# Kernel optimization log

Hardware: AMD Instinct MI355X
Metric: run time of the kernel (lower is better)

## Reference

```python
import jax, jax.numpy as jnp
import numpy as np

D_MODEL = 1024
N_HEADS = 16
HEAD_DIM = D_MODEL // N_HEADS
N_SCALES = 11
_D4 = jnp.array([0.4829629131445341, 0.8365163037378079, 0.2241438680420134, -0.1294095225512604], dtype=jnp.float32)


def setup_inputs() -> dict:
    key = jax.random.key(0)
    ks = jax.random.split(key, 8)
    B, N, D = 8, 2048, D_MODEL
    s = 1.0 / np.sqrt(D)
    x = jax.random.normal(ks[0], (B, N, D), dtype=jnp.float32)
    qkv_w = jax.random.normal(ks[1], (3 * D, D), dtype=jnp.float32) * s
    qkv_b = jnp.zeros((3 * D,), dtype=jnp.float32)
    out_w = jax.random.normal(ks[2], (D, D), dtype=jnp.float32) * s
    out_b = jnp.zeros((D,), dtype=jnp.float32)
    gate_w = jax.random.normal(ks[3], (D, D), dtype=jnp.float32) * s
    gate_b = jnp.full((D,), 2.0, dtype=jnp.float32)  # nn.init.constant_(gate_proj.bias, 2.0)
    scale_gain = jax.random.normal(ks[4], (N_SCALES, N_HEADS), dtype=jnp.float32) * 0.1
    field_coupling = jnp.eye(N_HEADS, dtype=jnp.float32) + 0.01 * jax.random.normal(ks[5], (N_HEADS, N_HEADS), dtype=jnp.float32)
    return {"x": x, "qkv_w": qkv_w, "qkv_b": qkv_b, "out_w": out_w, "out_b": out_b,
            "gate_w": gate_w, "gate_b": gate_b, "scale_gain": scale_gain,
            "field_coupling": field_coupling}


def _causal_multiscale(x_c, scale_gain):
    # x_c: [B, C, N] with channel order (head-major, then head_dim)
    B, C, N = x_c.shape
    gains = jax.nn.softmax(scale_gain, axis=0)              # [S, H]
    gains_exp = jnp.repeat(gains, HEAD_DIM, axis=1)         # [S, C]
    out = jnp.zeros_like(x_c)
    for j in range(N_SCALES):
        d = 1 << j
        xp = jnp.pad(x_c, ((0, 0), (0, 0), (3 * d, 0)))     # causal left pad
        # depthwise dilated conv (cross-correlation, same D4 taps per channel)
        y = (_D4[0] * xp[:, :, 0 * d:0 * d + N]
             + _D4[1] * xp[:, :, 1 * d:1 * d + N]
             + _D4[2] * xp[:, :, 2 * d:2 * d + N]
             + _D4[3] * xp[:, :, 3 * d:3 * d + N])
        out = out + gains_exp[j][None, :, None] * y
    return out


def reference(x, qkv_w, qkv_b, out_w, out_b, gate_w, gate_b, scale_gain, field_coupling):
    B, N, D = x.shape
    H, HD = N_HEADS, HEAD_DIM
    qkv = x @ qkv_w.T + qkv_b                               # [B, N, 3D]
    q, k, v = jnp.split(qkv, 3, axis=-1)                    # q is unused (as in source)
    k = k.reshape(B, N, H, HD)
    v = v.reshape(B, N, H, HD)
    k_mag = jnp.linalg.norm(k, axis=-1, keepdims=True)      # [B, N, H, 1]
    field = v * k_mag                                       # [B, N, H, HD]
    # -> [B, C, N], C = H*HD, head-major channel layout
    x_c = jnp.transpose(field, (0, 2, 3, 1)).reshape(B, H * HD, N)
    out_c = _causal_multiscale(x_c, scale_gain)             # [B, C, N]
    field = out_c.reshape(B, H, HD, N)                      # [B, H, HD, N]
    coupling = jax.nn.softmax(field_coupling, axis=-1)      # [H, H]
    field = jnp.einsum('ij,bjdn->bidn', coupling, field)    # head coupling
    gathered = jnp.transpose(field, (0, 3, 1, 2)).reshape(B, N, D)
    gate = jax.nn.sigmoid(x @ gate_w.T + gate_b)
    return (gathered * gate) @ out_w.T + out_b
```

## Files before the change

kernel.cpp:

```cpp
#include <hip/hip_runtime.h>
#include <hip/hip_bf16.h>
#include <math.h>

#define BD 8
#define SN 2048
#define DM 1024
#define NH 16
#define HD 64
#define NS 11
#define NTAP 24
#define PAD 3072

typedef __attribute__((ext_vector_type(8))) short short8;
typedef __attribute__((ext_vector_type(4))) float floatx4;

__constant__ int OFFS[NTAP] = {0, 1, 2, 3, 4, 6, 8, 12, 16, 24, 32, 48, 64, 96,
                               128, 192, 256, 384, 512, 768, 1024, 1536, 2048, 3072};

__device__ __forceinline__ void async_load16(const void* g, void* lds) {
    __builtin_amdgcn_global_load_lds(
        (const __attribute__((address_space(1))) void*)g,
        (__attribute__((address_space(3))) void*)lds,
        16, 0, 0);
}

__global__ __launch_bounds__(256) void f2bf_kernel(const float* __restrict__ src,
                                                   __hip_bfloat16* __restrict__ dst,
                                                   int n4) {
    int i = blockIdx.x * 256 + threadIdx.x;
    if (i < n4) {
        const float4 v = reinterpret_cast<const float4*>(src)[i];
        union { __hip_bfloat16 h[4]; uint2 u; } cv;
        cv.h[0] = __float2bfloat16(v.x);
        cv.h[1] = __float2bfloat16(v.y);
        cv.h[2] = __float2bfloat16(v.z);
        cv.h[3] = __float2bfloat16(v.w);
        reinterpret_cast<uint2*>(dst)[i] = cv.u;
    }
}

__global__ void prep_kernel(const float* __restrict__ scale_gain,
                            const float* __restrict__ field_coupling,
                            float* __restrict__ wtab,
                            float* __restrict__ cw) {
    const float D4[4] = {0.4829629131445341f, 0.8365163037378079f,
                         0.2241438680420134f, -0.1294095225512604f};
    int t = threadIdx.x;
    if (t < NH) {
        float g[NS];
        float m = -1e30f;
        for (int j = 0; j < NS; ++j) m = fmaxf(m, scale_gain[j * NH + t]);
        float s = 0.f;
        for (int j = 0; j < NS; ++j) { g[j] = expf(scale_gain[j * NH + t] - m); s += g[j]; }
        float inv = 1.f / s;
        for (int j = 0; j < NS; ++j) g[j] *= inv;
        for (int i = 0; i < NTAP; ++i) {
            float w = 0.f;
            for (int j = 0; j < NS; ++j)
                for (int tt = 0; tt < 4; ++tt)
                    if (((3 - tt) << j) == OFFS[i]) w += g[j] * D4[tt];
            wtab[i * NH + t] = w;
        }
    } else if (t < 2 * NH) {
        int r = t - NH;
        float m = -1e30f;
        for (int j = 0; j < NH; ++j) m = fmaxf(m, field_coupling[r * NH + j]);
        float e[NH]; float s = 0.f;
        for (int j = 0; j < NH; ++j) { e[j] = expf(field_coupling[r * NH + j] - m); s += e[j]; }
        float inv = 1.f / s;
        for (int j = 0; j < NH; ++j) cw[r * NH + j] = e[j] * inv;
    }
}

__global__ __launch_bounds__(256, 3) void gemm128_kernel(
    const __hip_bfloat16* __restrict__ A,
    const __hip_bfloat16* __restrict__ Bw,
    void* __restrict__ Cout,
    const float* __restrict__ bias,
    int M, int Nn, int K, int act, int bf16out) {
    __shared__ short As[128 * 64];
    __shared__ short Bs[128 * 64];

    const int tid = threadIdx.x;
    const int m0 = blockIdx.y * 128;
    const int n0 = blockIdx.x * 128;
    const int wv = tid >> 6;
    const int ln = tid & 63;

    const int srow = ln >> 3;
    const int scc  = (ln & 7) ^ srow;
    size_t goffA[4], goffB[4];
    #pragma unroll
    for (int i = 0; i < 4; ++i) {
        const int row = wv * 32 + i * 8 + srow;
        goffA[i] = (size_t)(m0 + row) * K + scc * 8;
        goffB[i] = (size_t)(n0 + row) * K + scc * 8;
    }

    const int lrow = ln & 15, quad = ln >> 4;
    const int wm = (wv >> 1) * 64;
    const int wn = (wv & 1) * 64;
    int aaddr[4], baddr[4];
    #pragma unroll
    for (int t = 0; t < 4; ++t) {
        const int sw = (quad ^ (lrow & 7)) * 16;
        aaddr[t] = (wm + t * 16 + lrow) * 128 + sw;
        baddr[t] = (wn + t * 16 + lrow) * 128 + sw;
    }

    floatx4 acc[4][4];
    #pragma unroll
    for (int a = 0; a < 4; ++a)
        #pragma unroll
        for (int b = 0; b < 4; ++b) acc[a][b] = (floatx4){0.f, 0.f, 0.f, 0.f};

    for (int kt = 0; kt < K; kt += 64) {
        #pragma unroll
        for (int i = 0; i < 4; ++i) {
            async_load16(A + goffA[i] + kt, &As[(wv * 32 + i * 8) * 64]);
            async_load16(Bw + goffB[i] + kt, &Bs[(wv * 32 + i * 8) * 64]);
        }
        __syncthreads();
        #pragma unroll
        for (int h = 0; h < 2; ++h) {
            short8 a[4], b[4];
            #pragma unroll
            for (int t = 0; t < 4; ++t) {
                a[t] = *reinterpret_cast<const short8*>(
                           reinterpret_cast<const char*>(As) + (aaddr[t] ^ (h * 64)));
                b[t] = *reinterpret_cast<const short8*>(
                           reinterpret_cast<const char*>(Bs) + (baddr[t] ^ (h * 64)));
            }
            #pragma unroll
            for (int mt = 0; mt < 4; ++mt)
                #pragma unroll
                for (int nt = 0; nt < 4; ++nt)
                    acc[mt][nt] = __builtin_amdgcn_mfma_f32_16x16x32_bf16(
                        a[mt], b[nt], acc[mt][nt], 0, 0, 0);
        }
        __syncthreads();
    }

    #pragma unroll
    for (int mt = 0; mt < 4; ++mt) {
        #pragma unroll
        for (int nt = 0; nt < 4; ++nt) {
            const int col = n0 + wn + nt * 16 + lrow;
            const float bv = bias ? bias[col] : 0.f;
            #pragma unroll
            for (int i = 0; i < 4; ++i) {
                const int row = m0 + wm + mt * 16 + quad * 4 + i;
                float val = acc[mt][nt][i] + bv;
                if (act == 1) val = 1.f / (1.f + expf(-val));
                if (bf16out)
                    ((__hip_bfloat16*)Cout)[(size_t)row * Nn + col] = __float2bfloat16(val);
                else
                    ((float*)Cout)[(size_t)row * Nn + col] = val;
            }
        }
    }
}

__global__ __launch_bounds__(256) void fieldize_kernel(const __hip_bfloat16* __restrict__ kv,
                                                       __hip_bfloat16* __restrict__ field) {
    const int b = blockIdx.z, h = blockIdx.y, n0 = blockIdx.x * 64;
    __shared__ float kt[64][65];
    __shared__ float vt[64][65];
    __shared__ float mag[64];
    const int t = threadIdx.x;
    #pragma unroll
    for (int i = 0; i < 16; ++i) {
        int idx = t + i * 256;
        int nl = idx >> 6, d = idx & 63;
        size_t rbase = (size_t)(b * SN + n0 + nl) * 2048;
        kt[nl][d] = __bfloat162float(kv[rbase + h * 64 + d]);
        vt[nl][d] = __bfloat162float(kv[rbase + 1024 + h * 64 + d]);
    }
    __syncthreads();
    if (t < 64) {
        float s = 0.f;
        #pragma unroll
        for (int d = 0; d < 64; ++d) { float x = kt[t][d]; s += x * x; }
        mag[t] = sqrtf(s);
    }
    __syncthreads();
    #pragma unroll
    for (int i = 0; i < 16; ++i) {
        int idx = t + i * 256;
        int d = idx >> 6, nl = idx & 63;
        field[((size_t)b * DM + h * 64 + d) * SN + n0 + nl] =
            __float2bfloat16(vt[nl][d] * mag[nl]);
    }
}

__global__ __launch_bounds__(256) void wavelet_kernel(const __hip_bfloat16* __restrict__ field,
                                                      const float* __restrict__ wtab,
                                                      __hip_bfloat16* __restrict__ wave) {
    const int bc = blockIdx.x;
    const int c = bc & (DM - 1);
    const int h = c >> 6;
    __shared__ float row[PAD + SN];
    __shared__ float wt[NTAP];
    const __hip_bfloat16* src = field + (size_t)bc * SN;
    const int t = threadIdx.x;
    for (int i = t; i < PAD; i += 256) row[i] = 0.f;
    for (int i = t; i < SN; i += 256) row[PAD + i] = __bfloat162float(src[i]);
    if (t < NTAP) wt[t] = wtab[t * NH + h];
    __syncthreads();
    __hip_bfloat16* dst = wave + (size_t)bc * SN;
    for (int n = t; n < SN; n += 256) {
        const float* base = &row[PAD + n];
        float acc = 0.f;
        #pragma unroll
        for (int i = 0; i < NTAP; ++i) acc += wt[i] * base[-OFFS[i]];
        dst[n] = __float2bfloat16(acc);
    }
}

__global__ __launch_bounds__(256) void couple_kernel(const __hip_bfloat16* __restrict__ wave,
                                                     const float* __restrict__ cw,
                                                     __hip_bfloat16* __restrict__ cpl) {
    const int b = blockIdx.z, d = blockIdx.y;
    const int n = blockIdx.x * 256 + threadIdx.x;
    __shared__ float w[256];
    w[threadIdx.x] = cw[threadIdx.x];
    __syncthreads();
    size_t base = (size_t)b * DM * SN + (size_t)d * SN + n;
    float r[NH];
    #pragma unroll
    for (int hi = 0; hi < NH; ++hi) r[hi] = __bfloat162float(wave[base + (size_t)hi * 64 * SN]);
    #pragma unroll
    for (int ho = 0; ho < NH; ++ho) {
        float acc = 0.f;
        #pragma unroll
        for (int hi = 0; hi < NH; ++hi) acc += w[ho * 16 + hi] * r[hi];
        cpl[base + (size_t)ho * 64 * SN] = __float2bfloat16(acc);
    }
}

__global__ __launch_bounds__(256) void transgate_kernel(const __hip_bfloat16* __restrict__ cpl,
                                                        const __hip_bfloat16* __restrict__ gate,
                                                        __hip_bfloat16* __restrict__ Ag) {
    const int b = blockIdx.z;
    const int c0 = blockIdx.y * 64, n0 = blockIdx.x * 64;
    __shared__ float tile[64][65];
    const int t = threadIdx.x;
    #pragma unroll
    for (int i = 0; i < 16; ++i) {
        int idx = t + i * 256;
        int ci = idx >> 6, nj = idx & 63;
        tile[ci][nj] = __bfloat162float(cpl[((size_t)b * DM + c0 + ci) * SN + n0 + nj]);
    }
    __syncthreads();
    #pragma unroll
    for (int i = 0; i < 16; ++i) {
        int idx = t + i * 256;
        int nj = idx >> 6, ci = idx & 63;
        size_t off = ((size_t)(b * SN + n0 + nj)) * DM + c0 + ci;
        Ag[off] = __float2bfloat16(tile[ci][nj] * __bfloat162float(gate[off]));
    }
}

extern "C" void kernel_launch(void* const* d_in, const int* in_sizes, int n_in,
                              void* d_out, int out_size, void* d_ws, size_t ws_size,
                              hipStream_t stream) {
    const float* x     = (const float*)d_in[0];
    const float* qkv_w = (const float*)d_in[1];
    const float* qkv_b = (const float*)d_in[2];
    const float* out_w = (const float*)d_in[3];
    const float* out_b = (const float*)d_in[4];
    const float* gate_w = (const float*)d_in[5];
    const float* gate_b = (const float*)d_in[6];
    const float* scale_gain = (const float*)d_in[7];
    const float* field_coupling = (const float*)d_in[8];

    char* ws = (char*)d_ws;
    const int M = BD * SN;

    __hip_bfloat16* x_bf   = (__hip_bfloat16*)(ws);
    __hip_bfloat16* wkv_bf = (__hip_bfloat16*)(ws + 33554432);
    __hip_bfloat16* wg_bf  = (__hip_bfloat16*)(ws + 37748736);
    __hip_bfloat16* wo_bf  = (__hip_bfloat16*)(ws + 39845888);
    float* wtab            = (float*)(ws + 41943040);
    float* cwbuf           = (float*)(ws + 41944576);
    __hip_bfloat16* gate_bf  = (__hip_bfloat16*)(ws + 41945600);
    __hip_bfloat16* field_bf = (__hip_bfloat16*)(ws + 75500032);
    __hip_bfloat16* wave_bf  = (__hip_bfloat16*)(ws + 109054464);
    __hip_bfloat16* kv_bf  = (__hip_bfloat16*)d_out;
    __hip_bfloat16* cpl_bf = field_bf;
    __hip_bfloat16* Ag     = x_bf;
    float* out = (float*)d_out;

    f2bf_kernel<<<(M * DM / 4 + 255) / 256, 256, 0, stream>>>(x, x_bf, M * DM / 4);
    f2bf_kernel<<<(2 * DM * DM / 4 + 255) / 256, 256, 0, stream>>>(qkv_w + (size_t)DM * DM, wkv_bf, 2 * DM * DM / 4);
    f2bf_kernel<<<(DM * DM / 4 + 255) / 256, 256, 0, stream>>>(gate_w, wg_bf, DM * DM / 4);
    f2bf_kernel<<<(DM * DM / 4 + 255) / 256, 256, 0, stream>>>(out_w, wo_bf, DM * DM / 4);

    prep_kernel<<<1, 64, 0, stream>>>(scale_gain, field_coupling, wtab, cwbuf);

    {
        dim3 grid(2 * DM / 128, M / 128);
        gemm128_kernel<<<grid, 256, 0, stream>>>(x_bf, wkv_bf, kv_bf, qkv_b + DM, M, 2 * DM, DM, 0, 1);
    }
    {
        dim3 grid(DM / 128, M / 128);
        gemm128_kernel<<<grid, 256, 0, stream>>>(x_bf, wg_bf, gate_bf, gate_b, M, DM, DM, 1, 1);
    }
    {
        dim3 grid(SN / 64, NH, BD);
        fieldize_kernel<<<grid, 256, 0, stream>>>(kv_bf, field_bf);
    }
    wavelet_kernel<<<BD * DM, 256, 0, stream>>>(field_bf, wtab, wave_bf);
    {
        dim3 grid(SN / 256, HD, BD);
        couple_kernel<<<grid, 256, 0, stream>>>(wave_bf, cwbuf, cpl_bf);
    }
    {
        dim3 grid(SN / 64, DM / 64, BD);
        transgate_kernel<<<grid, 256, 0, stream>>>(cpl_bf, gate_bf, Ag);
    }
    {
        dim3 grid(DM / 128, M / 128);
        gemm128_kernel<<<grid, 256, 0, stream>>>(Ag, wo_bf, out, out_b, M, DM, DM, 0, 0);
    }
}
```

Measured before the change: 417.3 us.

## Fuse K-norm into GEMM epilogue and compute V transposed directly

The K and gate projections are merged into one GEMM. Its epilogue reduces each head's K row to a norm with wave shuffles and writes only the per-row magnitude, so K is never stored. V is computed as a transposed GEMM (W_v · x^T) to produce the channel-major layout directly, and the magnitude multiply moves into the wavelet kernel's load. This removes the fieldize kernel and the intermediate KV round trip. The cost is an extra bias-concat step and a transposed GEMM whose output stores may be less coalesced.

Measured after the change: 409.1 us. -2.0%, faster.

```diff
diff --git a/kernel.cpp b/kernel.cpp
--- a/kernel.cpp
+++ b/kernel.cpp
@@ -41,8 +41,12 @@
 
 __global__ void prep_kernel(const float* __restrict__ scale_gain,
                             const float* __restrict__ field_coupling,
+                            const float* __restrict__ qkv_b,
+                            const float* __restrict__ gate_b,
                             float* __restrict__ wtab,
-                            float* __restrict__ cw) {
+                            float* __restrict__ cw,
+                            float* __restrict__ biascat)
+{
     const float D4[4] = {0.4829629131445341f, 0.8365163037378079f,
                          0.2241438680420134f, -0.1294095225512604f};
     int t = threadIdx.x;
@@ -70,6 +74,8 @@
         float inv = 1.f / s;
         for (int j = 0; j < NH; ++j) cw[r * NH + j] = e[j] * inv;
     }
+    for (int i = t; i < 2048; i += 256)
+        biascat[i] = (i < 1024) ? qkv_b[1024 + i] : gate_b[i - 1024];
 }
 
 __global__ __launch_bounds__(256, 3) void gemm128_kernel(
@@ -77,7 +83,8 @@
     const __hip_bfloat16* __restrict__ Bw,
     void* __restrict__ Cout,
     const float* __restrict__ bias,
-    int M, int Nn, int K, int act, int bf16out) {
+    float* __restrict__ kmag,
+    int M, int Nn, int K, int mode) {
     __shared__ short As[128 * 64];
     __shared__ short Bs[128 * 64];
 
@@ -141,70 +148,73 @@
         __syncthreads();
     }
 
+    if (mode == 2 && n0 < 1024) {
+        const int h = (n0 + wn) >> 6;
+        #pragma unroll
+        for (int mt = 0; mt < 4; ++mt) {
+            #pragma unroll
+            for (int i = 0; i < 4; ++i) {
+                float ss = 0.f;
+                #pragma unroll
+                for (int nt = 0; nt < 4; ++nt) {
+                    const float v = acc[mt][nt][i] + bias[n0 + wn + nt * 16 + lrow];
+                    ss += v * v;
+                }
+                ss += __shfl_xor(ss, 1);
+                ss += __shfl_xor(ss, 2);
+                ss += __shfl_xor(ss, 4);
+                ss += __shfl_xor(ss, 8);
+                if (lrow == 0) {
+                    const int r = m0 + wm + mt * 16 + quad * 4 + i;
+                    kmag[h * (BD * SN) + r] = sqrtf(ss);
+                }
+            }
+        }
+        return;
+    }
+
     #pragma unroll
     for (int mt = 0; mt < 4; ++mt) {
         #pragma unroll
         for (int nt = 0; nt < 4; ++nt) {
             const int col = n0 + wn + nt * 16 + lrow;
-            const float bv = bias ? bias[col] : 0.f;
+            float bv = 0.f;
+            if (bias && mode != 1) bv = bias[col];
             #pragma unroll
             for (int i = 0; i < 4; ++i) {
                 const int row = m0 + wm + mt * 16 + quad * 4 + i;
                 float val = acc[mt][nt][i] + bv;
-                if (act == 1) val = 1.f / (1.f + expf(-val));
-                if (bf16out)
+                if (mode == 1 && bias) val += bias[row];
+                if (mode == 0) {
+                    ((float*)Cout)[(size_t)row * Nn + col] = val;
+                } else if (mode == 1) {
                     ((__hip_bfloat16*)Cout)[(size_t)row * Nn + col] = __float2bfloat16(val);
-                else
-                    ((float*)Cout)[(size_t)row * Nn + col] = val;
+                } else {
+                    val = 1.f / (1.f + expf(-val));
+                    ((__hip_bfloat16*)Cout)[(size_t)row * 1024 + (col - 1024)] =
+                        __float2bfloat16(val);
+                }
             }
         }
     }
 }
 
-__global__ __launch_bounds__(256) void fieldize_kernel(const __hip_bfloat16* __restrict__ kv,
-                                                       __hip_bfloat16* __restrict__ field) {
-    const int b = blockIdx.z, h = blockIdx.y, n0 = blockIdx.x * 64;
-    __shared__ float kt[64][65];
-    __shared__ float vt[64][65];
-    __shared__ float mag[64];
-    const int t = threadIdx.x;
-    #pragma unroll
-    for (int i = 0; i < 16; ++i) {
-        int idx = t + i * 256;
-        int nl = idx >> 6, d = idx & 63;
-        size_t rbase = (size_t)(b * SN + n0 + nl) * 2048;
-        kt[nl][d] = __bfloat162float(kv[rbase + h * 64 + d]);
-        vt[nl][d] = __bfloat162float(kv[rbase + 1024 + h * 64 + d]);
-    }
-    __syncthreads();
-    if (t < 64) {
-        float s = 0.f;
-        #pragma unroll
-        for (int d = 0; d < 64; ++d) { float x = kt[t][d]; s += x * x; }
-        mag[t] = sqrtf(s);
-    }
-    __syncthreads();
-    #pragma unroll
-    for (int i = 0; i < 16; ++i) {
-        int idx = t + i * 256;
-        int d = idx >> 6, nl = idx & 63;
-        field[((size_t)b * DM + h * 64 + d) * SN + n0 + nl] =
-            __float2bfloat16(vt[nl][d] * mag[nl]);
-    }
-}
-
-__global__ __launch_bounds__(256) void wavelet_kernel(const __hip_bfloat16* __restrict__ field,
+__global__ __launch_bounds__(256) void wavelet_kernel(const __hip_bfloat16* __restrict__ fieldv,
+                                                      const float* __restrict__ kmag,
                                                       const float* __restrict__ wtab,
                                                       __hip_bfloat16* __restrict__ wave) {
     const int bc = blockIdx.x;
+    const int b = bc >> 10;
     const int c = bc & (DM - 1);
     const int h = c >> 6;
     __shared__ float row[PAD + SN];
     __shared__ float wt[NTAP];
-    const __hip_bfloat16* src = field + (size_t)bc * SN;
+    const __hip_bfloat16* src = fieldv + (size_t)c * (BD * SN) + b * SN;
+    const float* mag = kmag + (size_t)h * (BD * SN) + b * SN;
     const int t = threadIdx.x;
     for (int i = t; i < PAD; i += 256) row[i] = 0.f;
-    for (int i = t; i < SN; i += 256) row[PAD + i] = __bfloat162float(src[i]);
+    for (int i = t; i < SN; i += 256)
+        row[PAD + i] = __bfloat162float(src[i]) * mag[i];
     if (t < NTAP) wt[t] = wtab[t * NH + h];
     __syncthreads();
     __hip_bfloat16* dst = wave + (size_t)bc * SN;
@@ -277,40 +287,41 @@
     char* ws = (char*)d_ws;
     const int M = BD * SN;
 
-    __hip_bfloat16* x_bf   = (__hip_bfloat16*)(ws);
-    __hip_bfloat16* wkv_bf = (__hip_bfloat16*)(ws + 33554432);
-    __hip_bfloat16* wg_bf  = (__hip_bfloat16*)(ws + 37748736);
-    __hip_bfloat16* wo_bf  = (__hip_bfloat16*)(ws + 39845888);
-    float* wtab            = (float*)(ws + 41943040);
-    float* cwbuf           = (float*)(ws + 41944576);
-    __hip_bfloat16* gate_bf  = (__hip_bfloat16*)(ws + 41945600);
-    __hip_bfloat16* field_bf = (__hip_bfloat16*)(ws + 75500032);
-    __hip_bfloat16* wave_bf  = (__hip_bfloat16*)(ws + 109054464);
-    __hip_bfloat16* kv_bf  = (__hip_bfloat16*)d_out;
-    __hip_bfloat16* cpl_bf = field_bf;
+    __hip_bfloat16* x_bf    = (__hip_bfloat16*)(ws);
+    __hip_bfloat16* wkg_bf  = (__hip_bfloat16*)(ws + 33554432);
+    __hip_bfloat16* wv_bf   = (__hip_bfloat16*)(ws + 37748736);
+    __hip_bfloat16* wo_bf   = (__hip_bfloat16*)(ws + 39845888);
+    float* wtab             = (float*)(ws + 41943040);
+    float* cwbuf            = (float*)(ws + 41944576);
+    float* biascat          = (float*)(ws + 41945600);
+    float* kmag             = (float*)(ws + 41953792);
+    __hip_bfloat16* fieldv  = (__hip_bfloat16*)(ws + 43002368);
+    __hip_bfloat16* gate_bf = (__hip_bfloat16*)(ws + 76556800);
+    __hip_bfloat16* wave_bf = (__hip_bfloat16*)(ws + 110111232);
+    __hip_bfloat16* cpl_bf = fieldv;
     __hip_bfloat16* Ag     = x_bf;
     float* out = (float*)d_out;
 
     f2bf_kernel<<<(M * DM / 4 + 255) / 256, 256, 0, stream>>>(x, x_bf, M * DM / 4);
-    f2bf_kernel<<<(2 * DM * DM / 4 + 255) / 256, 256, 0, stream>>>(qkv_w + (size_t)DM * DM, wkv_bf, 2 * DM * DM / 4);
-    f2bf_kernel<<<(DM * DM / 4 + 255) / 256, 256, 0, stream>>>(gate_w, wg_bf, DM * DM / 4);
+    f2bf_kernel<<<(DM * DM / 4 + 255) / 256, 256, 0, stream>>>(qkv_w + (size_t)DM * DM, wkg_bf, DM * DM / 4);
+    f2bf_kernel<<<(DM * DM / 4 + 255) / 256, 256, 0, stream>>>(gate_w, wkg_bf + (size_t)DM * DM, DM * DM / 4);
+    f2bf_kernel<<<(DM * DM / 4 + 255) / 256, 256, 0, stream>>>(qkv_w + (size_t)2 * DM * DM, wv_bf, DM * DM / 4);
     f2bf_kernel<<<(DM * DM / 4 + 255) / 256, 256, 0, stream>>>(out_w, wo_bf, DM * DM / 4);
 
-    prep_kernel<<<1, 64, 0, stream>>>(scale_gain, field_coupling, wtab, cwbuf);
+    prep_kernel<<<1, 256, 0, stream>>>(scale_gain, field_coupling, qkv_b, gate_b,
+                                       wtab, cwbuf, biascat);
 
     {
         dim3 grid(2 * DM / 128, M / 128);
-        gemm128_kernel<<<grid, 256, 0, stream>>>(x_bf, wkv_bf, kv_bf, qkv_b + DM, M, 2 * DM, DM, 0, 1);
-    }
-    {
-        dim3 grid(DM / 128, M / 128);
-        gemm128_kernel<<<grid, 256, 0, stream>>>(x_bf, wg_bf, gate_bf, gate_b, M, DM, DM, 1, 1);
-    }
-    {
-        dim3 grid(SN / 64, NH, BD);
-        fieldize_kernel<<<grid, 256, 0, stream>>>(kv_bf, field_bf);
-    }
-    wavelet_kernel<<<BD * DM, 256, 0, stream>>>(field_bf, wtab, wave_bf);
+        gemm128_kernel<<<grid, 256, 0, stream>>>(x_bf, wkg_bf, gate_bf, biascat, kmag,
+                                                 M, 2 * DM, DM, 2);
+    }
+    {
+        dim3 grid(M / 128, DM / 128);
+        gemm128_kernel<<<grid, 256, 0, stream>>>(wv_bf, x_bf, fieldv, qkv_b + 2 * DM, nullptr,
+                                                 DM, M, DM, 1);
+    }
+    wavelet_kernel<<<BD * DM, 256, 0, stream>>>(fieldv, kmag, wtab, wave_bf);
     {
         dim3 grid(SN / 256, HD, BD);
         couple_kernel<<<grid, 256, 0, stream>>>(wave_bf, cwbuf, cpl_bf);
@@ -321,6 +332,7 @@
     }
     {
         dim3 grid(DM / 128, M / 128);
-        gemm128_kernel<<<grid, 256, 0, stream>>>(Ag, wo_bf, out, out_b, M, DM, DM, 0, 0);
-    }
-}
+        gemm128_kernel<<<grid, 256, 0, stream>>>(Ag, wo_bf, out, out_b, nullptr,
+                                                 M, DM, DM, 0);
+    }
+}
```
